# Optimization experiments

Hardware: AMD Instinct MI355X
Metric: run time of the kernel (lower is better)

## Reference

```python
import jax, jax.numpy as jnp
import numpy as np

B, S, D, H, E, K = 2, 1024, 1024, 512, 16, 4  # batch, seq, hidden, expert inter, n_experts, top_k
HS = 2 * H  # shared expert inter dim = num_shared_experts * moe_inter_dim


def silu(z):
    return z * jax.nn.sigmoid(z)


def setup_inputs() -> dict:
    key = jax.random.key(0)
    ks = jax.random.split(key, 8)
    sc = lambda fan_in: 1.0 / np.sqrt(fan_in)
    x = jax.random.normal(ks[0], (B, S, D), jnp.float32)
    gate_w = jax.random.normal(ks[1], (E, D), jnp.float32) * sc(D)
    ws_in = jax.random.normal(ks[2], (D, HS), jnp.float32) * sc(D)
    vs_in = jax.random.normal(ks[3], (D, HS), jnp.float32) * sc(D)
    ws_out = jax.random.normal(ks[4], (HS, D), jnp.float32) * sc(HS)
    e_win = jax.random.normal(ks[5], (E, D, H), jnp.float32) * sc(D)
    e_vin = jax.random.normal(ks[6], (E, D, H), jnp.float32) * sc(D)
    e_wout = jax.random.normal(ks[7], (E, H, D), jnp.float32) * sc(H)
    return {"x": x, "gate_w": gate_w, "ws_in": ws_in, "vs_in": vs_in,
            "ws_out": ws_out, "e_win": e_win, "e_vin": e_vin, "e_wout": e_wout}


def reference(x, gate_w, ws_in, vs_in, ws_out, e_win, e_vin, e_wout):
    b, s, d = x.shape
    T = b * s
    xf = x.reshape(T, d)

    # --- Gate (eval path: biases buffer is zero / unused) ---
    g = jax.nn.sigmoid(xf @ gate_w.T)                      # [T, E]
    topv, topi = jax.lax.top_k(g, K)                        # [T, K]
    wn = topv / jnp.sum(topv, axis=-1, keepdims=True)       # normalized top-k weights
    # sparse combine matrix [T, E]: zero for unrouted experts -> exact same math
    # as the original per-expert masked gather/scatter loop
    combine = jnp.zeros_like(g).at[jnp.arange(T)[:, None], topi].add(wn)

    # --- Routed experts (SwiGLU), batched over experts ---
    hin = jnp.einsum('td,edh->eth', xf, e_win)              # [E, T, H]
    vin = jnp.einsum('td,edh->eth', xf, e_vin)              # [E, T, H]
    h = silu(hin) * vin * combine.T[:, :, None]             # weight before down-proj
    routed = jnp.einsum('eth,ehd->td', h, e_wout)           # [T, D]

    # --- Shared expert (SwiGLU with inter = num_shared * moe_inter) ---
    shared = (silu(xf @ ws_in) * (xf @ vs_in)) @ ws_out     # [T, D]

    return (shared + routed).reshape(b, s, d)
```

## Files before the change

### kernel.cpp

```cpp
#include <hip/hip_runtime.h>
#include <hip/hip_bf16.h>
#include <math.h>

typedef __attribute__((ext_vector_type(4))) float f32x4;
typedef __attribute__((ext_vector_type(8))) short s16x8;
typedef __hip_bfloat16 bf16;

constexpr int TOK = 2048;
constexpr int DIM = 1024;
constexpr int HID = 512;
constexpr int NE  = 16;
constexpr int NK  = 4;
constexpr int NHS = 1024;
constexpr int NPAIR = TOK * NK;

constexpr int UP_GRID = 128 + 4 * 80;
constexpr int DN_GRID = 64 + 4 * 80;

#define MFMA(a, b, c) __builtin_amdgcn_mfma_f32_16x16x32_bf16(a, b, c, 0, 0, 0)

#define GLOAD_LDS(gp, lp)                                                        \
  __builtin_amdgcn_global_load_lds(                                              \
      (const __attribute__((address_space(1))) unsigned int*)(gp),               \
      (__attribute__((address_space(3))) unsigned int*)(lp), 16, 0, 0)

template <int CH>
static __device__ __forceinline__ void stage_p(const bf16* const* rp, int k0,
                                               bf16* lds, int tid) {
  int wid = tid >> 6;
#pragma unroll
  for (int i = 0; i < CH; ++i) {
    int c = i * 512 + tid;
    int row = c >> 3;
    int slot = c & 7;
    int j = slot ^ (row & 7);
    const bf16* g = rp[i] + k0 + j * 8;
    bf16* l = lds + (size_t)(i * 512 + wid * 64) * 8;
    GLOAD_LDS(g, l);
  }
}

static __device__ __forceinline__ s16x8 frag(const bf16* lds, int row, int kc) {
  return *(const s16x8*)(lds + row * 64 + ((kc ^ (row & 7)) << 3));
}

static __device__ __forceinline__ float b2f(short u) {
  union { unsigned int i; float f; } c;
  c.i = ((unsigned int)(unsigned short)u) << 16;
  return c.f;
}

struct bf16x4 { bf16 a, b, c, d; };


static __device__ __forceinline__ void tr_tile(const float* __restrict__ src,
                                               bf16* __restrict__ dst, int R, int C,
                                               int bx, int by, float t[32][33], int tid) {
  int tx = tid & 31, ty = tid >> 5;
  int c0 = bx * 32, r0 = by * 32;
#pragma unroll
  for (int i = 0; i < 32; i += 8) t[ty + i][tx] = src[(size_t)(r0 + ty + i) * C + c0 + tx];
  __syncthreads();
#pragma unroll
  for (int i = 0; i < 32; i += 8)
    dst[(size_t)(c0 + ty + i) * R + r0 + tx] = __float2bfloat16(t[tx][ty + i]);
}

__global__ __launch_bounds__(256) void prep1(const float* __restrict__ ws_in,
                                             const float* __restrict__ vs_in,
                                             const float* __restrict__ e_win,
                                             const float* __restrict__ e_vin,
                                             bf16* __restrict__ wsinT, bf16* __restrict__ vsinT,
                                             bf16* __restrict__ ewinT, bf16* __restrict__ evinT) {
  __shared__ float t[32][33];
  int bid = blockIdx.x, tid = threadIdx.x;
  if (bid < 1024) {
    tr_tile(ws_in, wsinT, DIM, NHS, bid & 31, bid >> 5, t, tid);
  } else if (bid < 2048) {
    int b = bid - 1024;
    tr_tile(vs_in, vsinT, DIM, NHS, b & 31, b >> 5, t, tid);
  } else if (bid < 10240) {
    int b = bid - 2048, e = b >> 9; b &= 511;
    tr_tile(e_win + (size_t)e * DIM * HID, ewinT + (size_t)e * DIM * HID,
            DIM, HID, b & 15, b >> 4, t, tid);
  } else {
    int b = bid - 10240, e = b >> 9; b &= 511;
    tr_tile(e_vin + (size_t)e * DIM * HID, evinT + (size_t)e * DIM * HID,
            DIM, HID, b & 15, b >> 4, t, tid);
  }
}

__global__ __launch_bounds__(256) void prep2(const float* __restrict__ ws_out,
                                             const float* __restrict__ e_wout,
                                             bf16* __restrict__ wsoutT,
                                             bf16* __restrict__ ewoutT) {
  __shared__ float t[32][33];
  int bid = blockIdx.x, tid = threadIdx.x;
  if (bid < 1024) {
    tr_tile(ws_out, wsoutT, NHS, DIM, bid & 31, bid >> 5, t, tid);
  } else {
    int b = bid - 1024, e = b >> 9; b &= 511;
    tr_tile(e_wout + (size_t)e * HID * DIM, ewoutT + (size_t)e * HID * DIM,
            HID, DIM, b & 31, b >> 5, t, tid);
  }
}


__global__ __launch_bounds__(256) void gate_scores(const float* __restrict__ x,
                                                   const float* __restrict__ gw,
                                                   bf16* __restrict__ xb,
                                                   float* __restrict__ scores) {
  int lane = threadIdx.x & 63, wid = threadIdx.x >> 6;
  int t = blockIdx.x * 4 + wid;
  const float* xr = x + (size_t)t * DIM + lane * 16;
  float4 x4[4];
#pragma unroll
  for (int q = 0; q < 4; ++q) x4[q] = *(const float4*)(xr + q * 4);
  {
    bf16* xo = xb + (size_t)t * DIM + lane * 16;
#pragma unroll
    for (int q = 0; q < 4; ++q) {
      bf16x4 o{__float2bfloat16(x4[q].x), __float2bfloat16(x4[q].y),
               __float2bfloat16(x4[q].z), __float2bfloat16(x4[q].w)};
      *reinterpret_cast<bf16x4*>(xo + q * 4) = o;
    }
  }
  float s[NE];
#pragma unroll
  for (int e = 0; e < NE; ++e) {
    const float* wr_ = gw + (size_t)e * DIM + lane * 16;
    float a = 0.f;
#pragma unroll
    for (int q = 0; q < 4; ++q) {
      float4 w4 = *(const float4*)(wr_ + q * 4);
      a += x4[q].x * w4.x + x4[q].y * w4.y + x4[q].z * w4.z + x4[q].w * w4.w;
    }
    s[e] = a;
  }
#pragma unroll
  for (int e = 0; e < NE; ++e)
#pragma unroll
    for (int off = 32; off; off >>= 1) s[e] += __shfl_xor(s[e], off);
  if (lane == 0) {
#pragma unroll
    for (int e = 0; e < NE; ++e) scores[(size_t)t * NE + e] = s[e];
  }
}

__global__ __launch_bounds__(256) void topk_hist(const float* __restrict__ scores,
                                                 int* __restrict__ topi,
                                                 float* __restrict__ topw,
                                                 int* __restrict__ counts) {
  __shared__ int h[NE];
  int tid = threadIdx.x;
  int t = blockIdx.x * 256 + tid;
  if (tid < NE) h[tid] = 0;
  __syncthreads();
  float g[NE];
  const float* sr = scores + (size_t)t * NE;
#pragma unroll
  for (int q = 0; q < 4; ++q) {
    float4 v = *(const float4*)(sr + q * 4);
    g[q * 4 + 0] = 1.f / (1.f + expf(-v.x));
    g[q * 4 + 1] = 1.f / (1.f + expf(-v.y));
    g[q * 4 + 2] = 1.f / (1.f + expf(-v.z));
    g[q * 4 + 3] = 1.f / (1.f + expf(-v.w));
  }
  unsigned used = 0;
  int bi[NK]; float bv[NK];
  float sum = 0.f;
#pragma unroll
  for (int j = 0; j < NK; ++j) {
    int best = 0; float v = -1e30f;
#pragma unroll
    for (int e = 0; e < NE; ++e)
      if (!((used >> e) & 1u) && g[e] > v) { v = g[e]; best = e; }
    used |= 1u << best; bi[j] = best; bv[j] = v; sum += v;
  }
  float inv = 1.f / sum;
#pragma unroll
  for (int j = 0; j < NK; ++j) {
    topi[t * NK + j] = bi[j];
    topw[t * NK + j] = bv[j] * inv;
    atomicAdd(&h[bi[j]], 1);
  }
  __syncthreads();
  if (tid < NE) atomicAdd(&counts[tid], h[tid]);
}

__global__ __launch_bounds__(64) void route_small(const int* __restrict__ counts,
                                                  int* __restrict__ offs,
                                                  int* __restrict__ segs,
                                                  int* __restrict__ nseg,
                                                  int* __restrict__ cursor) {
  if (threadIdx.x != 0) return;
  int o = 0;
#pragma unroll
  for (int e = 0; e < NE; ++e) { offs[e] = o; cursor[e * 32] = 0; o += counts[e]; }
  int s = 0;
  for (int e = 0; e < NE; ++e)
    for (int m = 0; m < counts[e]; m += 128) segs[s++] = (e << 16) | m;
  nseg[0] = s;
}

__global__ __launch_bounds__(256) void scatter_pairs(const int* __restrict__ topi,
                                                     const float* __restrict__ topw,
                                                     const int* __restrict__ offs,
                                                     int* __restrict__ cursor,
                                                     int* __restrict__ tok_list,
                                                     float* __restrict__ w_list,
                                                     int* __restrict__ pair_slot) {
  int p = blockIdx.x * 256 + threadIdx.x;
  if (p >= NPAIR) return;
  int e = topi[p];
  int rank = atomicAdd(&cursor[e * 32], 1);
  int slot = offs[e] + rank;
  tok_list[slot] = p >> 2;
  w_list[slot] = topw[p];
  pair_slot[p] = slot;
}


__global__ __launch_bounds__(512, 4) void up_all(
    const bf16* __restrict__ xb, const bf16* __restrict__ wsinT,
    const bf16* __restrict__ vsinT, const bf16* __restrict__ ewinT,
    const bf16* __restrict__ evinT, const int* __restrict__ tok_list,
    const float* __restrict__ w_list, const int* __restrict__ counts,
    const int* __restrict__ offs, const int* __restrict__ segs,
    const int* __restrict__ nseg, bf16* __restrict__ hsb,
    bf16* __restrict__ hre) {
  int bid = blockIdx.x;
  int j = (bid & 7) * (UP_GRID / 8) + (bid >> 3);
  int nj = 128 + 4 * nseg[0];
  if (j >= nj) return;
  int tid = threadIdx.x, lane = tid & 63, wid = tid >> 6;
  int wr = wid >> 2, wc = wid & 3;

  bool is_shared = (j < 128);
  int m0, n0, cnt = TOK, off_e = 0;
  const bf16 *w1, *w2;
  if (is_shared) {
    m0 = (j >> 3) * 128; n0 = j & 7;
    w1 = wsinT; w2 = vsinT;
  } else {
    int r = j - 128;
    int sv = segs[r >> 2]; n0 = r & 3;
    int e = sv >> 16; m0 = sv & 0xffff;
    cnt = counts[e]; off_e = offs[e];
    w1 = ewinT + (size_t)e * HID * DIM;
    w2 = evinT + (size_t)e * HID * DIM;
  }

  const bf16* ap[2]; const bf16* bp[4];
#pragma unroll
  for (int i = 0; i < 2; ++i) {
    int row = (i * 512 + tid) >> 3;
    int gr = is_shared ? (m0 + row) : tok_list[off_e + min(m0 + row, cnt - 1)];
    ap[i] = xb + (size_t)gr * DIM;
  }
#pragma unroll
  for (int i = 0; i < 4; ++i) {
    int r = (i * 512 + tid) >> 3;
    int ridx = n0 * 128 + (r >> 5) * 16 + (r & 15);
    bp[i] = ((r & 16) ? w2 : w1) + (size_t)ridx * DIM;
  }

  __shared__ alignas(16) bf16 As[128 * 64], Bs[256 * 64];
  f32x4 acc[4][4];
  f32x4 z4 = {0.f, 0.f, 0.f, 0.f};
#pragma unroll
  for (int m = 0; m < 4; ++m)
#pragma unroll
    for (int q = 0; q < 4; ++q) acc[m][q] = z4;

  for (int k0 = 0; k0 < DIM; k0 += 64) {
    __syncthreads();
    stage_p<2>(ap, k0, As, tid);
    stage_p<4>(bp, k0, Bs, tid);
    __syncthreads();
#pragma unroll
    for (int ks = 0; ks < 2; ++ks) {
      int r16 = lane & 15, kc = (ks << 2) + (lane >> 4);
      s16x8 a[4];
#pragma unroll
      for (int m = 0; m < 4; ++m) a[m] = frag(As, wr * 64 + m * 16 + r16, kc);
#pragma unroll
      for (int q = 0; q < 4; ++q) {
        s16x8 b = frag(Bs, wc * 64 + q * 16 + r16, kc);
#pragma unroll
        for (int m = 0; m < 4; ++m) acc[m][q] = MFMA(a[m], b, acc[m][q]);
      }
    }
  }
#pragma unroll
  for (int m = 0; m < 4; ++m)
#pragma unroll
    for (int q = 0; q < 4; q += 2) {
      int c = n0 * 128 + (wc * 2 + (q >> 1)) * 16 + (lane & 15);
#pragma unroll
      for (int i = 0; i < 4; ++i) {
        int r = wr * 64 + m * 16 + (lane >> 4) * 4 + i;
        float z = acc[m][q][i], v = acc[m][q + 1][i];
        float h = z / (1.f + __expf(-z)) * v;
        if (is_shared) {
          hsb[(size_t)(m0 + r) * NHS + c] = __float2bfloat16(h);
        } else {
          int gr = m0 + r;
          if (gr < cnt)
            hre[(size_t)(off_e + gr) * HID + c] =
                __float2bfloat16(h * w_list[off_e + gr]);
        }
      }
    }
}


__global__ __launch_bounds__(512, 4) void down_all(
    const bf16* __restrict__ hsb, const bf16* __restrict__ wsoutT,
    const bf16* __restrict__ hre, const bf16* __restrict__ ewoutT,
    const int* __restrict__ tok_list, const int* __restrict__ counts,
    const int* __restrict__ offs, const int* __restrict__ segs,
    const int* __restrict__ nseg, float* __restrict__ out,
    bf16* __restrict__ hrd) {
  int bid = blockIdx.x;
  int j = (bid & 7) * (DN_GRID / 8) + (bid >> 3);
  int nj = 64 + 4 * nseg[0];
  if (j >= nj) return;
  int tid = threadIdx.x, lane = tid & 63, wid = tid >> 6;
  int wr = wid >> 2, wc = wid & 3;

  bool is_shared = (j < 64);
  int m0, n0, cnt = TOK, off_e = 0, K, ldA, ldB;
  const bf16 *Abase, *Bbase;
  if (is_shared) {
    m0 = (j >> 2) * 128; n0 = j & 3;
    Abase = hsb; ldA = NHS; K = NHS;
    Bbase = wsoutT; ldB = NHS;
  } else {
    int r = j - 64;
    int sv = segs[r >> 2]; n0 = r & 3;
    int e = sv >> 16; m0 = sv & 0xffff;
    cnt = counts[e]; off_e = offs[e];
    Abase = hre + (size_t)off_e * HID; ldA = HID; K = HID;
    Bbase = ewoutT + (size_t)e * DIM * HID; ldB = HID;
  }

  const bf16* ap[2]; const bf16* bp[4];
#pragma unroll
  for (int i = 0; i < 2; ++i) {
    int row = (i * 512 + tid) >> 3;
    int gr = is_shared ? (m0 + row) : min(m0 + row, cnt - 1);
    ap[i] = Abase + (size_t)gr * ldA;
  }
#pragma unroll
  for (int i = 0; i < 4; ++i) {
    int r = (i * 512 + tid) >> 3;
    bp[i] = Bbase + (size_t)(n0 * 256 + r) * ldB;
  }

  __shared__ alignas(16) bf16 As[128 * 64], Bs[256 * 64];
  f32x4 acc[4][4];
  f32x4 z4 = {0.f, 0.f, 0.f, 0.f};
#pragma unroll
  for (int m = 0; m < 4; ++m)
#pragma unroll
    for (int q = 0; q < 4; ++q) acc[m][q] = z4;

  int NT = K / 64;
  for (int kt = 0; kt < NT; ++kt) {
    int k0 = kt * 64;
    __syncthreads();
    stage_p<2>(ap, k0, As, tid);
    stage_p<4>(bp, k0, Bs, tid);
    __syncthreads();
#pragma unroll
    for (int ks = 0; ks < 2; ++ks) {
      int r16 = lane & 15, kc = (ks << 2) + (lane >> 4);
      s16x8 a[4];
#pragma unroll
      for (int m = 0; m < 4; ++m) a[m] = frag(As, wr * 64 + m * 16 + r16, kc);
#pragma unroll
      for (int q = 0; q < 4; ++q) {
        s16x8 b = frag(Bs, wc * 64 + q * 16 + r16, kc);
#pragma unroll
        for (int m = 0; m < 4; ++m) acc[m][q] = MFMA(a[m], b, acc[m][q]);
      }
    }
  }
#pragma unroll
  for (int m = 0; m < 4; ++m)
#pragma unroll
    for (int q = 0; q < 4; ++q) {
      int c = n0 * 256 + wc * 64 + q * 16 + (lane & 15);
#pragma unroll
      for (int i = 0; i < 4; ++i) {
        int r = wr * 64 + m * 16 + (lane >> 4) * 4 + i;
        if (is_shared) {
          out[(size_t)(m0 + r) * DIM + c] = acc[m][q][i];
        } else {
          int gr = m0 + r;
          if (gr < cnt)
            hrd[(size_t)(off_e + gr) * DIM + c] = __float2bfloat16(acc[m][q][i]);
        }
      }
    }
}


__global__ __launch_bounds__(256) void finish_add(const bf16* __restrict__ hrd,
                                                  const int* __restrict__ pair_slot,
                                                  float* __restrict__ out) {
  int idx = blockIdx.x * 256 + threadIdx.x;
  int t = idx >> 7;
  int c0 = (idx & 127) * 8;
  int4 s4 = *(const int4*)(pair_slot + t * 4);
  float acc[8];
  float* o = out + (size_t)t * DIM + c0;
#pragma unroll
  for (int k = 0; k < 8; ++k) acc[k] = o[k];
  int sl[4] = {s4.x, s4.y, s4.z, s4.w};
#pragma unroll
  for (int j = 0; j < 4; ++j) {
    s16x8 v = *(const s16x8*)(hrd + (size_t)sl[j] * DIM + c0);
#pragma unroll
    for (int k = 0; k < 8; ++k) acc[k] += b2f(v[k]);
  }
#pragma unroll
  for (int k = 0; k < 8; ++k) o[k] = acc[k];
}


extern "C" void kernel_launch(void* const* d_in, const int* in_sizes, int n_in,
                              void* d_out, int out_size, void* d_ws, size_t ws_size,
                              hipStream_t stream) {
  const float* x      = (const float*)d_in[0];
  const float* gw     = (const float*)d_in[1];
  const float* ws_in  = (const float*)d_in[2];
  const float* vs_in  = (const float*)d_in[3];
  const float* ws_out = (const float*)d_in[4];
  const float* e_win  = (const float*)d_in[5];
  const float* e_vin  = (const float*)d_in[6];
  const float* e_wout = (const float*)d_in[7];
  float* out = (float*)d_out;

  char* p = (char*)d_ws;
  bf16* xb     = (bf16*)p;  p += (size_t)TOK * DIM * 2;
  bf16* wsinT  = (bf16*)p;
  bf16* wsoutT = wsinT;
  p += (size_t)NHS * DIM * 2;
  bf16* vsinT  = (bf16*)p;  p += (size_t)NHS * DIM * 2;
  bf16* hsb    = (bf16*)p;  p += (size_t)TOK * NHS * 2;
  bf16* ewinT  = (bf16*)p;
  bf16* ewoutT = ewinT;
  p += (size_t)NE * DIM * HID * 2;
  bf16* evinT  = (bf16*)p;
  bf16* hrd    = evinT;
  p += (size_t)NE * DIM * HID * 2;
  bf16* hre    = (bf16*)p;  p += (size_t)(NPAIR + 128) * HID * 2;
  int*   topi      = (int*)p;    p += (size_t)NPAIR * 4;
  float* topw      = (float*)p;  p += (size_t)NPAIR * 4;
  int*   tok_list  = (int*)p;    p += (size_t)NPAIR * 4;
  float* w_list    = (float*)p;  p += (size_t)NPAIR * 4;
  int*   pair_slot = (int*)p;    p += (size_t)NPAIR * 4;
  float* scores    = (float*)p;  p += (size_t)TOK * NE * 4;
  int*   counts    = (int*)p;    p += 64;
  int*   offs      = (int*)p;    p += 64;
  int*   cursor    = (int*)p;    p += NE * 32 * 4;
  int*   segs      = (int*)p;    p += 128 * 4;
  int*   nseg      = (int*)p;    p += 64;

  hipMemsetAsync(counts, 0, NE * sizeof(int), stream);
  gate_scores<<<TOK / 4, 256, 0, stream>>>(x, gw, xb, scores);
  topk_hist<<<TOK / 256, 256, 0, stream>>>(scores, topi, topw, counts);
  route_small<<<1, 64, 0, stream>>>(counts, offs, segs, nseg, cursor);
  scatter_pairs<<<NPAIR / 256, 256, 0, stream>>>(topi, topw, offs, cursor,
                                                 tok_list, w_list, pair_slot);

  prep1<<<18432, 256, 0, stream>>>(ws_in, vs_in, e_win, e_vin,
                                   wsinT, vsinT, ewinT, evinT);

  up_all<<<UP_GRID, 512, 0, stream>>>(xb, wsinT, vsinT, ewinT, evinT, tok_list,
                                      w_list, counts, offs, segs, nseg, hsb, hre);

  prep2<<<9216, 256, 0, stream>>>(ws_out, e_wout, wsoutT, ewoutT);

  down_all<<<DN_GRID, 512, 0, stream>>>(hsb, wsoutT, hre, ewoutT, tok_list,
                                        counts, offs, segs, nseg, out, hrd);
  finish_add<<<TOK * DIM / 8 / 256, 256, 0, stream>>>(hrd, pair_slot, out);
}
```

Measured before the change: 143.8 us.

## Halve GEMM M-tile to 64 rows and double-buffer LDS with async prefetch

Both up and down grouped GEMM kernels move from 128-row tiles with a 2x4 warp grid to 64-row tiles with warps split along N only. Routed segments are cut into 64-token pieces, so the grids grow and less padding is wasted on partly filled expert segments. The K loop now double-buffers LDS and prefetches the tile two steps ahead, using manual vmcnt waits and barriers so global-to-LDS loads overlap the MFMAs. In exchange, each block reuses its B tile across fewer rows, and the hand-written waitcnt counts must match the number of loads issued per stage.

```diff
diff --git a/kernel.cpp b/kernel.cpp
--- a/kernel.cpp
+++ b/kernel.cpp
@@ -14,8 +14,8 @@
 constexpr int NHS = 1024;
 constexpr int NPAIR = TOK * NK;
 
-constexpr int UP_GRID = 128 + 4 * 80;
-constexpr int DN_GRID = 64 + 4 * 80;
+constexpr int UP_GRID = 256 + 4 * 144;
+constexpr int DN_GRID = 128 + 4 * 144;
 
 #define MFMA(a, b, c) __builtin_amdgcn_mfma_f32_16x16x32_bf16(a, b, c, 0, 0, 0)
 
@@ -199,7 +199,7 @@
   for (int e = 0; e < NE; ++e) { offs[e] = o; cursor[e * 32] = 0; o += counts[e]; }
   int s = 0;
   for (int e = 0; e < NE; ++e)
-    for (int m = 0; m < counts[e]; m += 128) segs[s++] = (e << 16) | m;
+    for (int m = 0; m < counts[e]; m += 64) segs[s++] = (e << 16) | m;
   nseg[0] = s;
 }
 
@@ -231,19 +231,18 @@
     bf16* __restrict__ hre) {
   int bid = blockIdx.x;
   int j = (bid & 7) * (UP_GRID / 8) + (bid >> 3);
-  int nj = 128 + 4 * nseg[0];
+  int nj = 256 + 4 * nseg[0];
   if (j >= nj) return;
-  int tid = threadIdx.x, lane = tid & 63, wid = tid >> 6;
-  int wr = wid >> 2, wc = wid & 3;
-
-  bool is_shared = (j < 128);
+  int tid = threadIdx.x, lane = tid & 63, w = tid >> 6;
+
+  bool is_shared = (j < 256);
   int m0, n0, cnt = TOK, off_e = 0;
   const bf16 *w1, *w2;
   if (is_shared) {
-    m0 = (j >> 3) * 128; n0 = j & 7;
+    m0 = (j >> 3) * 64; n0 = j & 7;
     w1 = wsinT; w2 = vsinT;
   } else {
-    int r = j - 128;
+    int r = j - 256;
     int sv = segs[r >> 2]; n0 = r & 3;
     int e = sv >> 16; m0 = sv & 0xffff;
     cnt = counts[e]; off_e = offs[e];
@@ -251,12 +250,11 @@
     w2 = evinT + (size_t)e * HID * DIM;
   }
 
-  const bf16* ap[2]; const bf16* bp[4];
-#pragma unroll
-  for (int i = 0; i < 2; ++i) {
-    int row = (i * 512 + tid) >> 3;
+  const bf16* ap[1]; const bf16* bp[4];
+  {
+    int row = tid >> 3;
     int gr = is_shared ? (m0 + row) : tok_list[off_e + min(m0 + row, cnt - 1)];
-    ap[i] = xb + (size_t)gr * DIM;
+    ap[0] = xb + (size_t)gr * DIM;
   }
 #pragma unroll
   for (int i = 0; i < 4; ++i) {
@@ -265,51 +263,62 @@
     bp[i] = ((r & 16) ? w2 : w1) + (size_t)ridx * DIM;
   }
 
-  __shared__ alignas(16) bf16 As[128 * 64], Bs[256 * 64];
-  f32x4 acc[4][4];
+  __shared__ alignas(16) bf16 As[2][64 * 64], Bs[2][256 * 64];
+  f32x4 acc[4][2];
   f32x4 z4 = {0.f, 0.f, 0.f, 0.f};
 #pragma unroll
-  for (int m = 0; m < 4; ++m)
-#pragma unroll
-    for (int q = 0; q < 4; ++q) acc[m][q] = z4;
-
-  for (int k0 = 0; k0 < DIM; k0 += 64) {
-    __syncthreads();
-    stage_p<2>(ap, k0, As, tid);
-    stage_p<4>(bp, k0, Bs, tid);
-    __syncthreads();
+  for (int m = 0; m < 4; ++m) { acc[m][0] = z4; acc[m][1] = z4; }
+
+  constexpr int NT = DIM / 64;
+  stage_p<1>(ap, 0, As[0], tid);
+  stage_p<4>(bp, 0, Bs[0], tid);
+  stage_p<1>(ap, 64, As[1], tid);
+  stage_p<4>(bp, 64, Bs[1], tid);
+
+  for (int kt = 0; kt < NT; ++kt) {
+    int cur = kt & 1;
+    if (kt + 1 < NT) asm volatile("s_waitcnt vmcnt(5)" ::: "memory");
+    else             asm volatile("s_waitcnt vmcnt(0)" ::: "memory");
+    __builtin_amdgcn_sched_barrier(0);
+    __builtin_amdgcn_s_barrier();
+    __builtin_amdgcn_sched_barrier(0);
+    const bf16* Ac = As[cur]; const bf16* Bc = Bs[cur];
 #pragma unroll
     for (int ks = 0; ks < 2; ++ks) {
       int r16 = lane & 15, kc = (ks << 2) + (lane >> 4);
       s16x8 a[4];
 #pragma unroll
-      for (int m = 0; m < 4; ++m) a[m] = frag(As, wr * 64 + m * 16 + r16, kc);
-#pragma unroll
-      for (int q = 0; q < 4; ++q) {
-        s16x8 b = frag(Bs, wc * 64 + q * 16 + r16, kc);
+      for (int m = 0; m < 4; ++m) a[m] = frag(Ac, m * 16 + r16, kc);
+#pragma unroll
+      for (int q = 0; q < 2; ++q) {
+        s16x8 b = frag(Bc, w * 32 + q * 16 + r16, kc);
 #pragma unroll
         for (int m = 0; m < 4; ++m) acc[m][q] = MFMA(a[m], b, acc[m][q]);
       }
     }
-  }
+    __builtin_amdgcn_s_barrier();
+    __builtin_amdgcn_sched_barrier(0);
+    if (kt + 2 < NT) {
+      stage_p<1>(ap, (kt + 2) * 64, As[cur], tid);
+      stage_p<4>(bp, (kt + 2) * 64, Bs[cur], tid);
+    }
+  }
+
+  int c = n0 * 128 + w * 16 + (lane & 15);
 #pragma unroll
   for (int m = 0; m < 4; ++m)
 #pragma unroll
-    for (int q = 0; q < 4; q += 2) {
-      int c = n0 * 128 + (wc * 2 + (q >> 1)) * 16 + (lane & 15);
-#pragma unroll
-      for (int i = 0; i < 4; ++i) {
-        int r = wr * 64 + m * 16 + (lane >> 4) * 4 + i;
-        float z = acc[m][q][i], v = acc[m][q + 1][i];
-        float h = z / (1.f + __expf(-z)) * v;
-        if (is_shared) {
-          hsb[(size_t)(m0 + r) * NHS + c] = __float2bfloat16(h);
-        } else {
-          int gr = m0 + r;
-          if (gr < cnt)
-            hre[(size_t)(off_e + gr) * HID + c] =
-                __float2bfloat16(h * w_list[off_e + gr]);
-        }
+    for (int i = 0; i < 4; ++i) {
+      int r = m * 16 + (lane >> 4) * 4 + i;
+      float z = acc[m][0][i], v = acc[m][1][i];
+      float h = z / (1.f + __expf(-z)) * v;
+      if (is_shared) {
+        hsb[(size_t)(m0 + r) * NHS + c] = __float2bfloat16(h);
+      } else {
+        int gr = m0 + r;
+        if (gr < cnt)
+          hre[(size_t)(off_e + gr) * HID + c] =
+              __float2bfloat16(h * w_list[off_e + gr]);
       }
     }
 }
@@ -324,20 +333,19 @@
     bf16* __restrict__ hrd) {
   int bid = blockIdx.x;
   int j = (bid & 7) * (DN_GRID / 8) + (bid >> 3);
-  int nj = 64 + 4 * nseg[0];
+  int nj = 128 + 4 * nseg[0];
   if (j >= nj) return;
-  int tid = threadIdx.x, lane = tid & 63, wid = tid >> 6;
-  int wr = wid >> 2, wc = wid & 3;
-
-  bool is_shared = (j < 64);
+  int tid = threadIdx.x, lane = tid & 63, w = tid >> 6;
+
+  bool is_shared = (j < 128);
   int m0, n0, cnt = TOK, off_e = 0, K, ldA, ldB;
   const bf16 *Abase, *Bbase;
   if (is_shared) {
-    m0 = (j >> 2) * 128; n0 = j & 3;
+    m0 = (j >> 2) * 64; n0 = j & 3;
     Abase = hsb; ldA = NHS; K = NHS;
     Bbase = wsoutT; ldB = NHS;
   } else {
-    int r = j - 64;
+    int r = j - 128;
     int sv = segs[r >> 2]; n0 = r & 3;
     int e = sv >> 16; m0 = sv & 0xffff;
     cnt = counts[e]; off_e = offs[e];
@@ -345,12 +353,11 @@
     Bbase = ewoutT + (size_t)e * DIM * HID; ldB = HID;
   }
 
-  const bf16* ap[2]; const bf16* bp[4];
-#pragma unroll
-  for (int i = 0; i < 2; ++i) {
-    int row = (i * 512 + tid) >> 3;
+  const bf16* ap[1]; const bf16* bp[4];
+  {
+    int row = tid >> 3;
     int gr = is_shared ? (m0 + row) : min(m0 + row, cnt - 1);
-    ap[i] = Abase + (size_t)gr * ldA;
+    ap[0] = Abase + (size_t)gr * ldA;
   }
 #pragma unroll
   for (int i = 0; i < 4; ++i) {
@@ -358,43 +365,55 @@
     bp[i] = Bbase + (size_t)(n0 * 256 + r) * ldB;
   }
 
-  __shared__ alignas(16) bf16 As[128 * 64], Bs[256 * 64];
-  f32x4 acc[4][4];
+  __shared__ alignas(16) bf16 As[2][64 * 64], Bs[2][256 * 64];
+  f32x4 acc[4][2];
   f32x4 z4 = {0.f, 0.f, 0.f, 0.f};
 #pragma unroll
-  for (int m = 0; m < 4; ++m)
-#pragma unroll
-    for (int q = 0; q < 4; ++q) acc[m][q] = z4;
+  for (int m = 0; m < 4; ++m) { acc[m][0] = z4; acc[m][1] = z4; }
 
   int NT = K / 64;
+  stage_p<1>(ap, 0, As[0], tid);
+  stage_p<4>(bp, 0, Bs[0], tid);
+  stage_p<1>(ap, 64, As[1], tid);
+  stage_p<4>(bp, 64, Bs[1], tid);
+
   for (int kt = 0; kt < NT; ++kt) {
-    int k0 = kt * 64;
-    __syncthreads();
-    stage_p<2>(ap, k0, As, tid);
-    stage_p<4>(bp, k0, Bs, tid);
-    __syncthreads();
+    int cur = kt & 1;
+    if (kt + 1 < NT) asm volatile("s_waitcnt vmcnt(5)" ::: "memory");
+    else             asm volatile("s_waitcnt vmcnt(0)" ::: "memory");
+    __builtin_amdgcn_sched_barrier(0);
+    __builtin_amdgcn_s_barrier();
+    __builtin_amdgcn_sched_barrier(0);
+    const bf16* Ac = As[cur]; const bf16* Bc = Bs[cur];
 #pragma unroll
     for (int ks = 0; ks < 2; ++ks) {
       int r16 = lane & 15, kc = (ks << 2) + (lane >> 4);
       s16x8 a[4];
 #pragma unroll
-      for (int m = 0; m < 4; ++m) a[m] = frag(As, wr * 64 + m * 16 + r16, kc);
-#pragma unroll
-      for (int q = 0; q < 4; ++q) {
-        s16x8 b = frag(Bs, wc * 64 + q * 16 + r16, kc);
+      for (int m = 0; m < 4; ++m) a[m] = frag(Ac, m * 16 + r16, kc);
+#pragma unroll
+      for (int q = 0; q < 2; ++q) {
+        s16x8 b = frag(Bc, w * 32 + q * 16 + r16, kc);
 #pragma unroll
         for (int m = 0; m < 4; ++m) acc[m][q] = MFMA(a[m], b, acc[m][q]);
       }
     }
-  }
-#pragma unroll
-  for (int m = 0; m < 4; ++m)
-#pragma unroll
-    for (int q = 0; q < 4; ++q) {
-      int c = n0 * 256 + wc * 64 + q * 16 + (lane & 15);
+    __builtin_amdgcn_s_barrier();
+    __builtin_amdgcn_sched_barrier(0);
+    if (kt + 2 < NT) {
+      stage_p<1>(ap, (kt + 2) * 64, As[cur], tid);
+      stage_p<4>(bp, (kt + 2) * 64, Bs[cur], tid);
+    }
+  }
+
+#pragma unroll
+  for (int q = 0; q < 2; ++q) {
+    int c = n0 * 256 + w * 32 + q * 16 + (lane & 15);
+#pragma unroll
+    for (int m = 0; m < 4; ++m)
 #pragma unroll
       for (int i = 0; i < 4; ++i) {
-        int r = wr * 64 + m * 16 + (lane >> 4) * 4 + i;
+        int r = m * 16 + (lane >> 4) * 4 + i;
         if (is_shared) {
           out[(size_t)(m0 + r) * DIM + c] = acc[m][q][i];
         } else {
@@ -403,7 +422,7 @@
             hrd[(size_t)(off_e + gr) * DIM + c] = __float2bfloat16(acc[m][q][i]);
         }
       }
-    }
+  }
 }
 
 
@@ -466,7 +485,7 @@
   int*   counts    = (int*)p;    p += 64;
   int*   offs      = (int*)p;    p += 64;
   int*   cursor    = (int*)p;    p += NE * 32 * 4;
-  int*   segs      = (int*)p;    p += 128 * 4;
+  int*   segs      = (int*)p;    p += 256 * 4;
   int*   nseg      = (int*)p;    p += 64;
 
   hipMemsetAsync(counts, 0, NE * sizeof(int), stream);
```

After: 153.5 us. 6.7% more time.
